# Kernel tuning notes

Hardware: AMD Instinct MI355X
Metric: run time of the kernel (lower is better)

Reference implementation:

```python
import jax, jax.numpy as jnp
import numpy as np

N_BINS = 32
R = 1.2
BOUND = 50.0
_m = N_BINS // 2
_x1L = BOUND * (R - 1.0) / (R ** _m - 1.0)
X1L = _x1L / (2.0 * BOUND)  # x1L rescaled to the [0,1] domain
_idx = np.arange(N_BINS + 1, dtype=np.float64) - _m
_xr = np.where(_idx >= 0, (1.0 - R ** _idx) / (1.0 - R), (1.0 - R ** np.abs(_idx)) / (1.0 - R))
_xr = np.where(_idx >= 0, _x1L * _xr, -_x1L * _xr)
_xr = (_xr + BOUND) / (2.0 * BOUND)
MESH = np.concatenate([[0.0], _xr[1:-1], [1.0]]).astype(np.float32)   # (n_bins+1,)
ESIZE = (MESH[1:] - MESH[:-1]).astype(np.float32)                     # (n_bins,)

N, D = 524288, 64

def setup_inputs() -> dict:
    key = jax.random.key(0)
    k1, k2, k3, k4 = jax.random.split(key, 4)
    return {
        "x": jax.random.normal(k1, (N, D), jnp.float32) * 5.0,
        "logdet": jnp.zeros((N, 1), jnp.float32),
        "p": jax.random.normal(k2, (N_BINS - 1, D), jnp.float32) * 0.1,
        "b": jax.random.normal(k3, (1, D), jnp.float32) * 0.1,
        "logs": jax.random.normal(k4, (1, D), jnp.float32) * 0.1,
    }

def reference(x, logdet, p, b, logs):
    mesh = jnp.asarray(MESH)              # (n_bins+1,)
    es = jnp.asarray(ESIZE)               # (n_bins,)
    # ---- actnorm (data_init already done; b_init = logs_init = 0) ----
    ls = jnp.clip(logs, -5.0, 5.0)
    z = (x + b) * jnp.exp(ls)             # (N, D)
    logdet = logdet + jnp.sum(ls)
    # ---- pdf normalization ----
    ep = jnp.exp(p)                                         # (n_bins-1, D)
    w = ((es[:-1] + es[1:]) / 2.0)[:, None]                 # trapezoid weights
    px = ep * ((1.0 - es[0]) / jnp.sum(ep * w, 0, keepdims=True))
    ones = jnp.ones((1, p.shape[1]), p.dtype)
    pdf = jnp.concatenate([ones, px, ones], 0)              # (n_bins+1, D)
    cell = (pdf[:-1] + pdf[1:]) / 2.0 * es[:, None]         # (n_bins, D)
    F_ref = jnp.concatenate([jnp.zeros_like(ones), jnp.cumsum(cell, 0)[:-1]], 0)  # (n_bins, D)
    # ---- forward CDF: analytic bin index + batched gather + quadratic interp ----
    xs = (z + BOUND) / (2.0 * BOUND)                        # map to [0,1]
    sgn = jnp.sign(xs - 0.5)
    mfl = jnp.floor(jnp.log(jnp.abs(xs - 0.5) * (R - 1.0) / X1L + 1.0) / np.log(R))
    k = jnp.where(sgn >= 0, N_BINS // 2 + mfl, N_BINS // 2 - mfl - 1).astype(jnp.int32)
    cover = (k * (k - (N_BINS - 1))) <= 0                   # inside the mesh?
    k = jnp.clip(k, 0, N_BINS - 1)
    v1 = jnp.take_along_axis(pdf, k, 0)                     # pdf at left node
    v2 = jnp.take_along_axis(pdf, k + 1, 0)                 # pdf at right node
    xmodi = xs - mesh[k]
    h = es[k]
    F_pre = jnp.take_along_axis(F_ref, k, 0)
    y = jnp.where(cover, F_pre + xmodi * xmodi * 0.5 * (v2 - v1) / h + xmodi * v1, xs)
    dlog = jnp.where(cover, xmodi * (v2 - v1) / h + v1, 1.0)
    logdet = logdet + jnp.sum(jnp.log(dlog), axis=1, keepdims=True)
    out = y * 2.0 * BOUND - BOUND
    return out, logdet
```

## Files before the change

### kernel.cpp

```cpp
#include <hip/hip_runtime.h>
#include <math.h>

#define NBINS 32
#define DCOLS 64
#define BLOCK 512

typedef float f32x4 __attribute__((ext_vector_type(4)));

#define WS_TAB   0
#define WS_S     8192
#define WS_T     8256
#define WS_SUMLS 8320

__device__ __forceinline__ int swz(int d) { return ((d & 3) << 4) | (d >> 2); }

__global__ __launch_bounds__(64) void precompute_kernel(
    const float* __restrict__ p, const float* __restrict__ b,
    const float* __restrict__ logs, float* __restrict__ ws)
{
  const int d = threadIdx.x;
  const int ds = swz(d);

  double powr[17];
  {
    double rp = 1.0;
    for (int i = 0; i <= 16; i++) { powr[i] = rp; rp *= 1.2; }
  }
  const double x1L = 50.0 * 0.2 / (powr[16] - 1.0);
  float meshf[NBINS + 1];
  for (int i = 0; i <= NBINS; i++) {
    int idx = i - 16;
    int a = idx >= 0 ? idx : -idx;
    double xr = (1.0 - powr[a]) / (1.0 - 1.2);
    xr = (idx >= 0) ? x1L * xr : -x1L * xr;
    meshf[i] = (float)((xr + 50.0) / 100.0);
  }
  meshf[0] = 0.0f;
  meshf[NBINS] = 1.0f;
  float esf[NBINS];
  for (int i = 0; i < NBINS; i++) esf[i] = meshf[i + 1] - meshf[i];

  float ls = logs[d];
  ls = fminf(fmaxf(ls, -5.0f), 5.0f);
  const float s = expf(ls);
  const float bd = b[d];

  float ep[NBINS - 1];
  float denom = 0.0f;
  for (int j = 0; j < NBINS - 1; j++) {
    ep[j] = expf(p[j * DCOLS + d]);
    denom += ep[j] * ((esf[j] + esf[j + 1]) * 0.5f);
  }
  const float fnorm = (1.0f - esf[0]) / denom;
  float pdf[NBINS + 1];
  pdf[0] = 1.0f;
  pdf[NBINS] = 1.0f;
  for (int j = 0; j < NBINS - 1; j++) pdf[j + 1] = ep[j] * fnorm;

  float F = 0.0f;
  for (int k = 0; k < NBINS; k++) {
    const double v1 = (double)pdf[k];
    const double v2 = (double)pdf[k + 1];
    const double h  = (double)esf[k];
    const double m  = (double)meshf[k];
    const double c2 = 0.5 * (v2 - v1) / h;
    const double c1 = v1;
    const double A  = (double)F - c1 * m + c2 * m * m;
    const double B  = c1 - 2.0 * c2 * m;
    const int slot = (k * DCOLS + ds) * 4;
    ws[WS_TAB + slot + 0] = (float)A;
    ws[WS_TAB + slot + 1] = (float)B;
    ws[WS_TAB + slot + 2] = (float)c2;
    ws[WS_TAB + slot + 3] = 0.0f;
    const float cell = 0.5f * (pdf[k] + pdf[k + 1]) * esf[k];
    F += cell;
  }

  ws[WS_S + d] = (float)((double)s * 0.01);
  ws[WS_T + d] = (float)((double)bd * (double)s * 0.01 + 0.5);

  float sum = ls;
  for (int m = 1; m < 64; m <<= 1) sum += __shfl_xor(sum, m, 64);
  if (d == 0) ws[WS_SUMLS] = sum;
}

__device__ __forceinline__ void proc4(
    const float4 xv, const float4 S4, const float4 T4,
    const float4* __restrict__ sT, int cg, float C1, float INVL2R,
    f32x4& res, float& lsum)
{
  float xs_[4] = { fmaf(xv.x, S4.x, T4.x), fmaf(xv.y, S4.y, T4.y),
                   fmaf(xv.z, S4.z, T4.z), fmaf(xv.w, S4.w, T4.w) };
  float r_[4];
  float ls = 0.0f;
#pragma unroll
  for (int i = 0; i < 4; i++) {
    const float xs = xs_[i];
    const float a  = fabsf(xs - 0.5f);
    const float u  = __log2f(fmaf(a, C1, 1.0f)) * INVL2R;
    const float mfl = floorf(u);
    const float kf  = (xs >= 0.5f) ? (16.0f + mfl) : (15.0f - mfl);
    const int k = (int)kf;
    const bool cover = (k >= 0) && (k <= NBINS - 1);
    const int kc = k < 0 ? 0 : (k > NBINS - 1 ? NBINS - 1 : k);
    const float4 co = sT[kc * DCOLS + 16 * i + cg];
    const float t  = fmaf(xs, co.z, co.y);
    const float y  = cover ? fmaf(xs, t, co.x) : xs;
    const float dl = fmaf(xs, co.z, t);
    r_[i] = fmaf(y, 100.0f, -50.0f);
    ls += cover ? __log2f(dl) : 0.0f;
  }
  res = (f32x4){r_[0], r_[1], r_[2], r_[3]};
  lsum += ls;
}

__global__ __launch_bounds__(BLOCK, 8) void fwd_kernel(
    const float* __restrict__ x, const float* __restrict__ logdet_in,
    const float* __restrict__ ws, float* __restrict__ out,
    float* __restrict__ logdet_out, int nrows, float C1, float INVL2R)
{
  __shared__ float4 sT[NBINS * DCOLS];
  {
    const float4* wsv = (const float4*)(ws);
    for (int i = threadIdx.x; i < NBINS * DCOLS; i += BLOCK)
      sT[i] = wsv[i];
  }
  const int lane = threadIdx.x & 63;
  const int wid  = threadIdx.x >> 6;
  const int cg   = lane & 15;
  const int rs   = lane >> 4;
  const int c0   = cg * 4;
  const float4 S4 = *(const float4*)(ws + WS_S + c0);
  const float4 T4 = *(const float4*)(ws + WS_T + c0);
  const float sumls = ws[WS_SUMLS];
  __syncthreads();

  const int gw = blockIdx.x * 8 + wid;
  const int nw = gridDim.x * 8;

  for (int r0 = gw * 16; r0 < nrows; r0 += nw * 16) {
    const int rA = r0 + rs;
    const int rB = r0 + 4 + rs;
    const int rC = r0 + 8 + rs;
    const int rD = r0 + 12 + rs;
    const float4 xA = *(const float4*)(x + (size_t)rA * DCOLS + c0);
    const float4 xB = *(const float4*)(x + (size_t)rB * DCOLS + c0);
    const float4 xC = *(const float4*)(x + (size_t)rC * DCOLS + c0);
    const float4 xD = *(const float4*)(x + (size_t)rD * DCOLS + c0);

    f32x4 res;
    float lA = 0.0f, lB = 0.0f, lC = 0.0f, lD = 0.0f;
    proc4(xA, S4, T4, sT, cg, C1, INVL2R, res, lA);
    __builtin_nontemporal_store(res, (f32x4*)(out + (size_t)rA * DCOLS + c0));
    proc4(xB, S4, T4, sT, cg, C1, INVL2R, res, lB);
    __builtin_nontemporal_store(res, (f32x4*)(out + (size_t)rB * DCOLS + c0));
    proc4(xC, S4, T4, sT, cg, C1, INVL2R, res, lC);
    __builtin_nontemporal_store(res, (f32x4*)(out + (size_t)rC * DCOLS + c0));
    proc4(xD, S4, T4, sT, cg, C1, INVL2R, res, lD);
    __builtin_nontemporal_store(res, (f32x4*)(out + (size_t)rD * DCOLS + c0));

#pragma unroll
    for (int m = 1; m < 16; m <<= 1) {
      lA += __shfl_xor(lA, m, 64);
      lB += __shfl_xor(lB, m, 64);
      lC += __shfl_xor(lC, m, 64);
      lD += __shfl_xor(lD, m, 64);
    }
    if (cg == 0) {
      const float LN2 = 0.6931471805599453f;
      logdet_out[rA] = logdet_in[rA] + sumls + LN2 * lA;
      logdet_out[rB] = logdet_in[rB] + sumls + LN2 * lB;
      logdet_out[rC] = logdet_in[rC] + sumls + LN2 * lC;
      logdet_out[rD] = logdet_in[rD] + sumls + LN2 * lD;
    }
  }
}

extern "C" void kernel_launch(void* const* d_in, const int* in_sizes, int n_in,
                              void* d_out, int out_size, void* d_ws, size_t ws_size,
                              hipStream_t stream) {
  const float* x      = (const float*)d_in[0];
  const float* logdet = (const float*)d_in[1];
  const float* p      = (const float*)d_in[2];
  const float* b      = (const float*)d_in[3];
  const float* logs   = (const float*)d_in[4];
  float* out = (float*)d_out;
  float* ws  = (float*)d_ws;

  const int N = in_sizes[0] / DCOLS;
  float* logdet_out = out + (size_t)N * DCOLS;

  precompute_kernel<<<1, 64, 0, stream>>>(p, b, logs, ws);

  double Rm = 1.0;
  for (int i = 0; i < 16; i++) Rm *= 1.2;
  const double x1L = 50.0 * (1.2 - 1.0) / (Rm - 1.0);
  const double X1L = x1L / 100.0;
  const float C1      = (float)((1.2 - 1.0) / X1L);
  const float INVL2R  = (float)(1.0 / log2(1.2));

  const int grid = 1024;
  fwd_kernel<<<grid, BLOCK, 0, stream>>>(x, logdet, ws, out, logdet_out, N,
                                         C1, INVL2R);
}
```

Before: 250.1 us.

## Double-buffer x tiles into LDS via async global_load_lds prefetch

Replaces direct per-thread global loads of x with per-wave double-buffered asynchronous global-to-LDS copies. The next 8-row tile is prefetched while the current one is processed, using explicit waitcnt and a fixed iteration count. The grid is resized so each wave handles exactly NITER tiles, and the occupancy hint drops from 8 to 4. The aim is to hide memory latency, but the bounds check is removed so N must be a multiple of the tile product, and the hand-written vmcnt counts are fragile.

```diff
diff --git a/kernel.cpp b/kernel.cpp
--- a/kernel.cpp
+++ b/kernel.cpp
@@ -4,6 +4,9 @@
 #define NBINS 32
 #define DCOLS 64
 #define BLOCK 512
+#define NWAVES_BLK 8
+#define TILE_ROWS 8
+#define NITER 8
 
 typedef float f32x4 __attribute__((ext_vector_type(4)));
 
@@ -13,6 +16,12 @@
 #define WS_SUMLS 8320
 
 __device__ __forceinline__ int swz(int d) { return ((d & 3) << 4) | (d >> 2); }
+
+typedef __attribute__((address_space(1))) const void gv_t;
+typedef __attribute__((address_space(3))) void lv_t;
+__device__ __forceinline__ void gld_lds16(const void* g, void* l) {
+  __builtin_amdgcn_global_load_lds((gv_t*)g, (lv_t*)l, 16, 0, 0);
+}
 
 __global__ __launch_bounds__(64) void precompute_kernel(
     const float* __restrict__ p, const float* __restrict__ b,
@@ -114,12 +123,13 @@
   lsum += ls;
 }
 
-__global__ __launch_bounds__(BLOCK, 8) void fwd_kernel(
+__global__ __launch_bounds__(BLOCK, 4) void fwd_kernel(
     const float* __restrict__ x, const float* __restrict__ logdet_in,
     const float* __restrict__ ws, float* __restrict__ out,
-    float* __restrict__ logdet_out, int nrows, float C1, float INVL2R)
+    float* __restrict__ logdet_out, float C1, float INVL2R)
 {
   __shared__ float4 sT[NBINS * DCOLS];
+  __shared__ float  sX[NWAVES_BLK][2][TILE_ROWS * DCOLS];
   {
     const float4* wsv = (const float4*)(ws);
     for (int i = threadIdx.x; i < NBINS * DCOLS; i += BLOCK)
@@ -135,43 +145,61 @@
   const float sumls = ws[WS_SUMLS];
   __syncthreads();
 
-  const int gw = blockIdx.x * 8 + wid;
-  const int nw = gridDim.x * 8;
-
-  for (int r0 = gw * 16; r0 < nrows; r0 += nw * 16) {
-    const int rA = r0 + rs;
-    const int rB = r0 + 4 + rs;
-    const int rC = r0 + 8 + rs;
-    const int rD = r0 + 12 + rs;
-    const float4 xA = *(const float4*)(x + (size_t)rA * DCOLS + c0);
-    const float4 xB = *(const float4*)(x + (size_t)rB * DCOLS + c0);
-    const float4 xC = *(const float4*)(x + (size_t)rC * DCOLS + c0);
-    const float4 xD = *(const float4*)(x + (size_t)rD * DCOLS + c0);
+  const int gw = blockIdx.x * NWAVES_BLK + wid;
+  const int NW = gridDim.x * NWAVES_BLK;
+
+  float* xbuf0 = &sX[wid][0][0];
+  float* xbuf1 = &sX[wid][1][0];
+
+  {
+    const float* g0 = x + (size_t)gw * TILE_ROWS * DCOLS;
+    gld_lds16(g0 + lane * 4,       xbuf0);
+    gld_lds16(g0 + 256 + lane * 4, xbuf0 + 256);
+  }
+
+  const float LN2 = 0.6931471805599453f;
+
+#pragma unroll
+  for (int t = 0; t < NITER; ++t) {
+    const size_t r0 = ((size_t)t * NW + gw) * TILE_ROWS;
+    const int    tn = (t + 1 < NITER) ? (t + 1) : t;
+    const size_t rN = ((size_t)tn * NW + gw) * TILE_ROWS;
+    float* cbuf = (t & 1) ? xbuf1 : xbuf0;
+    float* nbuf = (t & 1) ? xbuf0 : xbuf1;
+
+    const float ldA = logdet_in[r0 + rs];
+    const float ldB = logdet_in[r0 + 4 + rs];
+
+    asm volatile("s_waitcnt lgkmcnt(0)" ::: "memory");
+
+    {
+      const float* gn = x + rN * DCOLS;
+      gld_lds16(gn + lane * 4,       nbuf);
+      gld_lds16(gn + 256 + lane * 4, nbuf + 256);
+    }
+
+    if (t == 0) asm volatile("s_waitcnt vmcnt(4)" ::: "memory");
+    else        asm volatile("s_waitcnt vmcnt(8)" ::: "memory");
+    __builtin_amdgcn_sched_barrier(0);
+
+    const float4 xA = *(const float4*)(cbuf + (size_t)rs * DCOLS + c0);
+    const float4 xB = *(const float4*)(cbuf + (size_t)(4 + rs) * DCOLS + c0);
 
     f32x4 res;
-    float lA = 0.0f, lB = 0.0f, lC = 0.0f, lD = 0.0f;
+    float lA = 0.0f, lB = 0.0f;
     proc4(xA, S4, T4, sT, cg, C1, INVL2R, res, lA);
-    __builtin_nontemporal_store(res, (f32x4*)(out + (size_t)rA * DCOLS + c0));
+    __builtin_nontemporal_store(res, (f32x4*)(out + (r0 + rs) * DCOLS + c0));
     proc4(xB, S4, T4, sT, cg, C1, INVL2R, res, lB);
-    __builtin_nontemporal_store(res, (f32x4*)(out + (size_t)rB * DCOLS + c0));
-    proc4(xC, S4, T4, sT, cg, C1, INVL2R, res, lC);
-    __builtin_nontemporal_store(res, (f32x4*)(out + (size_t)rC * DCOLS + c0));
-    proc4(xD, S4, T4, sT, cg, C1, INVL2R, res, lD);
-    __builtin_nontemporal_store(res, (f32x4*)(out + (size_t)rD * DCOLS + c0));
+    __builtin_nontemporal_store(res, (f32x4*)(out + (r0 + 4 + rs) * DCOLS + c0));
 
 #pragma unroll
     for (int m = 1; m < 16; m <<= 1) {
       lA += __shfl_xor(lA, m, 64);
       lB += __shfl_xor(lB, m, 64);
-      lC += __shfl_xor(lC, m, 64);
-      lD += __shfl_xor(lD, m, 64);
     }
     if (cg == 0) {
-      const float LN2 = 0.6931471805599453f;
-      logdet_out[rA] = logdet_in[rA] + sumls + LN2 * lA;
-      logdet_out[rB] = logdet_in[rB] + sumls + LN2 * lB;
-      logdet_out[rC] = logdet_in[rC] + sumls + LN2 * lC;
-      logdet_out[rD] = logdet_in[rD] + sumls + LN2 * lD;
+      logdet_out[r0 + rs]     = ldA + sumls + LN2 * lA;
+      logdet_out[r0 + 4 + rs] = ldB + sumls + LN2 * lB;
     }
   }
 }
@@ -199,7 +227,7 @@
   const float C1      = (float)((1.2 - 1.0) / X1L);
   const float INVL2R  = (float)(1.0 / log2(1.2));
 
-  const int grid = 1024;
-  fwd_kernel<<<grid, BLOCK, 0, stream>>>(x, logdet, ws, out, logdet_out, N,
+  const int grid = N / (NWAVES_BLK * TILE_ROWS * NITER);
+  fwd_kernel<<<grid, BLOCK, 0, stream>>>(x, logdet, ws, out, logdet_out,
                                          C1, INVL2R);
 }
```

Result: no change. 250.2 us (+0.0%).
